# Kernel tuning notes

Hardware: AMD Instinct MI355X
Metric: run time of the kernel (lower is better)

The kernel has to match this reference:

```python
import jax, jax.numpy as jnp
import numpy as np
from jax import lax

B, C, H, W = 8, 512, 16, 16
Di, N, R, K = 1024, 16, 32, 4  # d_inner, d_state, dt_rank, num scan directions
EPS = 1e-5


def _ln(x, g, b):
    mu = x.mean(-1, keepdims=True)
    var = ((x - mu) ** 2).mean(-1, keepdims=True)
    return (x - mu) * lax.rsqrt(var + EPS) * g + b


def _ss2d_core(xc, x_proj_w, dt_w, dt_b, A_logs, Ds):
    # xc: (b, Di, H, W) after depthwise conv + SiLU. 4-direction selective scan.
    b = xc.shape[0]
    L = H * W
    x_flat = xc.reshape(b, Di, L)
    x_wh = xc.transpose(0, 1, 3, 2).reshape(b, Di, L)
    x_hwwh = jnp.stack([x_flat, x_wh], 1)                  # (b,2,Di,L)
    xs = jnp.concatenate([x_hwwh, x_hwwh[..., ::-1]], 1)   # (b,K,Di,L)
    x_dbl = jnp.einsum('bkdl,kcd->bkcl', xs, x_proj_w)     # (b,K,R+2N,L)
    dts, Bs, Cs = x_dbl[:, :, :R], x_dbl[:, :, R:R + N], x_dbl[:, :, R + N:]
    dts = jnp.einsum('bkrl,kdr->bkdl', dts, dt_w)
    delta = jax.nn.softplus(dts + dt_b[None, :, :, None])  # (b,K,Di,L)
    A = -jnp.exp(A_logs).reshape(K, Di, N)                 # (K,Di,N)

    def step(h, inp):
        d, u, Bl, Cl = inp  # d,u:(b,K,Di)  Bl,Cl:(b,K,N)
        h = jnp.exp(d[..., None] * A) * h + (d * u)[..., None] * Bl[:, :, None, :]
        yl = jnp.einsum('bkdn,bkn->bkd', h, Cl)
        return h, yl

    inps = (delta.transpose(3, 0, 1, 2), xs.transpose(3, 0, 1, 2),
            Bs.transpose(3, 0, 1, 2), Cs.transpose(3, 0, 1, 2))
    h0 = jnp.zeros((b, K, Di, N), xc.dtype)
    _, ys = lax.scan(step, h0, inps)                       # (L,b,K,Di)
    ys = ys.transpose(1, 2, 3, 0) + xs * Ds.reshape(1, K, Di, 1)  # + D*u skip
    inv = ys[:, 2:4, :, ::-1]
    wh = ys[:, 1].reshape(b, Di, W, H).transpose(0, 1, 3, 2).reshape(b, Di, L)
    invwh = inv[:, 1].reshape(b, Di, W, H).transpose(0, 1, 3, 2).reshape(b, Di, L)
    y = ys[:, 0] + inv[:, 0] + wh + invwh                  # (b,Di,L)
    return y.transpose(0, 2, 1).reshape(b, H, W, Di)


def _conv_ffn(x, ffn_conv_w, bn_g, bn_b, bn_mean, bn_var, fc1_w, fc2_w):
    x = lax.conv_general_dilated(x, ffn_conv_w, (1, 1), [(1, 1), (1, 1)],
                                 dimension_numbers=('NCHW', 'OIHW', 'NCHW'))
    x = ((x - bn_mean[:, None, None]) * lax.rsqrt(bn_var + EPS)[:, None, None]
         * bn_g[:, None, None] + bn_b[:, None, None])
    x = jnp.clip(x, 0.0, 6.0)                              # ReLU6
    x = jnp.einsum('bchw,oc->bohw', x, fc1_w)              # 1x1 conv fc1
    x = jax.nn.gelu(x, approximate=False)
    return jnp.einsum('bchw,oc->bohw', x, fc2_w)           # 1x1 conv fc2


def _forward(x, y, ln1_g, ln1_b, in_proj_w, conv_w, conv_b, x_proj_w, dt_w,
             dt_b, A_logs, Ds, out_norm_g, out_norm_b, out_proj_w, ffn_conv_w,
             bn_g, bn_b, bn_mean, bn_var, fc1_w, fc2_w, lin1_w, lin1_b,
             lin2_w, lin2_b):
    # --- VSSBlock: LN -> SS2D -> residual ---
    x1 = x.transpose(0, 2, 3, 1)                           # (B,H,W,C)
    xn = _ln(x1, ln1_g, ln1_b)
    xz = jnp.einsum('bhwc,oc->bhwo', xn, in_proj_w)        # in_proj (no bias)
    xa, z = xz[..., :Di], xz[..., Di:]
    xc = xa.transpose(0, 3, 1, 2)                          # (B,Di,H,W)
    xc = lax.conv_general_dilated(xc, conv_w, (1, 1), [(1, 1), (1, 1)],
                                  feature_group_count=Di,
                                  dimension_numbers=('NCHW', 'OIHW', 'NCHW'))
    xc = jax.nn.silu(xc + conv_b[:, None, None])
    yc = _ss2d_core(xc, x_proj_w, dt_w, dt_b, A_logs, Ds)  # (B,H,W,Di)
    yc = _ln(yc, out_norm_g, out_norm_b) * jax.nn.silu(z)
    vss = x1 + jnp.einsum('bhwd,od->bhwo', yc, out_proj_w)
    # --- ConvFFN ---
    xm = _conv_ffn(vss.transpose(0, 3, 1, 2), ffn_conv_w, bn_g, bn_b, bn_mean,
                   bn_var, fc1_w, fc2_w)                   # (B,C,H,W)
    # --- channel attention: both pools are AdaptiveAvgPool2d(1), so max==avg ---
    pooled = y.mean(axis=(2, 3))                           # (B,C)
    lin = jax.nn.relu(pooled @ lin1_w.T + lin1_b) @ lin2_w.T + lin2_b
    gate = jax.nn.sigmoid(2.0 * lin)                       # linear_max + linear_avg
    return gate[:, :, None, None] * xm


def setup_inputs() -> dict:
    key = jax.random.key(0)
    ks = jax.random.split(key, 16)
    n = lambda i, shape, s=0.05: jax.random.normal(ks[i], shape, jnp.float32) * s
    return {
        'x': n(0, (B, C, H, W), 1.0),
        'y': n(1, (B, C, H, W), 1.0),
        'ln1_g': jnp.ones((C,), jnp.float32), 'ln1_b': jnp.zeros((C,), jnp.float32),
        'in_proj_w': n(2, (2 * Di, C)),
        'conv_w': n(3, (Di, 1, 3, 3), 0.2), 'conv_b': jnp.zeros((Di,), jnp.float32),
        'x_proj_w': n(4, (K, R + 2 * N, Di)),
        'dt_w': n(5, (K, Di, R), 0.1), 'dt_b': n(6, (K, Di), 0.1),
        'A_logs': n(7, (K * Di, N), 0.1), 'Ds': jnp.ones((K * Di,), jnp.float32),
        'out_norm_g': jnp.ones((Di,), jnp.float32), 'out_norm_b': jnp.zeros((Di,), jnp.float32),
        'out_proj_w': n(8, (C, Di)),
        'ffn_conv_w': n(9, (C, C, 3, 3)),
        'bn_g': jnp.ones((C,), jnp.float32), 'bn_b': jnp.zeros((C,), jnp.float32),
        'bn_mean': jnp.zeros((C,), jnp.float32), 'bn_var': jnp.ones((C,), jnp.float32),
        'fc1_w': n(10, (C, C)), 'fc2_w': n(11, (C, C)),
        'lin1_w': n(12, (C // 2, C)), 'lin1_b': jnp.zeros((C // 2,), jnp.float32),
        'lin2_w': n(13, (C, C // 2)), 'lin2_b': jnp.zeros((C,), jnp.float32),
    }


def reference(x, y, ln1_g, ln1_b, in_proj_w, conv_w, conv_b, x_proj_w, dt_w,
              dt_b, A_logs, Ds, out_norm_g, out_norm_b, out_proj_w, ffn_conv_w,
              bn_g, bn_b, bn_mean, bn_var, fc1_w, fc2_w, lin1_w, lin1_b,
              lin2_w, lin2_b):
    return _forward(x, y, ln1_g, ln1_b, in_proj_w, conv_w, conv_b, x_proj_w,
                    dt_w, dt_b, A_logs, Ds, out_norm_g, out_norm_b, out_proj_w,
                    ffn_conv_w, bn_g, bn_b, bn_mean, bn_var, fc1_w, fc2_w,
                    lin1_w, lin1_b, lin2_w, lin2_b)
```

## Files before the change

kernel.cpp:

```cpp
#include <hip/hip_runtime.h>
#include <hip/hip_bf16.h>
#include <math.h>

#define DEV_INLINE __device__ __forceinline__

constexpr int B_ = 8, C_ = 512, L_ = 256;
constexpr float EPS_ = 1e-5f;

typedef __attribute__((ext_vector_type(8))) short bf16x8;
typedef __attribute__((ext_vector_type(4))) float f32x4;

DEV_INLINE int lmap1(int l) { return ((l & 15) << 4) | (l >> 4); }
DEV_INLINE float sigmoidf_(float x) { return 1.f / (1.f + __expf(-x)); }
DEV_INLINE float siluf_(float x) { return x * sigmoidf_(x); }
DEV_INLINE float ex2_(float x) { return __builtin_amdgcn_exp2f(x); }

DEV_INLINE unsigned pk2(float a, float b) {
    __hip_bfloat16 x = __float2bfloat16(a), y = __float2bfloat16(b);
    unsigned short ux = *reinterpret_cast<unsigned short*>(&x);
    unsigned short uy = *reinterpret_cast<unsigned short*>(&y);
    return ((unsigned)uy << 16) | ux;
}

__global__ __launch_bounds__(256) void k_pool(const float* __restrict__ y, float* __restrict__ pooled) {
    int bc = blockIdx.x;
    int t = threadIdx.x;
    __shared__ float red[256];
    red[t] = y[bc * 256 + t];
    __syncthreads();
    for (int s = 128; s > 0; s >>= 1) { if (t < s) red[t] += red[t + s]; __syncthreads(); }
    if (t == 0) pooled[bc] = red[0] * (1.f / 256.f);
}

__global__ __launch_bounds__(256) void k_gate(const float* __restrict__ pooled,
                                              const float* __restrict__ lin1_w, const float* __restrict__ lin1_b,
                                              const float* __restrict__ lin2_w, const float* __restrict__ lin2_b,
                                              float* __restrict__ gate) {
    int b = blockIdx.x;
    int t = threadIdx.x;
    __shared__ float p[512];
    __shared__ float h1[256];
    p[t] = pooled[b * 512 + t];
    p[t + 256] = pooled[b * 512 + t + 256];
    __syncthreads();
    float s = lin1_b[t];
    const float4* wp1 = (const float4*)(lin1_w + t * 512);
    #pragma unroll 4
    for (int c = 0; c < 128; ++c) {
        float4 pv = *(const float4*)(p + c * 4);
        float4 wv = wp1[c];
        s = fmaf(pv.x, wv.x, s); s = fmaf(pv.y, wv.y, s);
        s = fmaf(pv.z, wv.z, s); s = fmaf(pv.w, wv.w, s);
    }
    h1[t] = fmaxf(s, 0.f);
    __syncthreads();
    #pragma unroll
    for (int cc = 0; cc < 2; ++cc) {
        int c = t + cc * 256;
        float s2 = lin2_b[c];
        const float4* wp2 = (const float4*)(lin2_w + c * 256);
        #pragma unroll 4
        for (int j = 0; j < 64; ++j) {
            float4 hv = *(const float4*)(h1 + j * 4);
            float4 wv = wp2[j];
            s2 = fmaf(hv.x, wv.x, s2); s2 = fmaf(hv.y, wv.y, s2);
            s2 = fmaf(hv.z, wv.z, s2); s2 = fmaf(hv.w, wv.w, s2);
        }
        gate[b * 512 + c] = sigmoidf_(2.f * s2);
    }
}

__global__ __launch_bounds__(256) void k_ln(const float* __restrict__ x, const float* __restrict__ g,
                                            const float* __restrict__ bta, __hip_bfloat16* __restrict__ xnb) {
    int pos = blockIdx.x;
    int b = pos >> 8, l = pos & 255;
    int t = threadIdx.x;
    float v0 = x[(b * C_ + t) * L_ + l];
    float v1 = x[(b * C_ + t + 256) * L_ + l];
    __shared__ float red[256];
    red[t] = v0 + v1;
    __syncthreads();
    for (int s = 128; s > 0; s >>= 1) { if (t < s) red[t] += red[t + s]; __syncthreads(); }
    float mu = red[0] * (1.f / 512.f);
    __syncthreads();
    float d0 = v0 - mu, d1 = v1 - mu;
    red[t] = d0 * d0 + d1 * d1;
    __syncthreads();
    for (int s = 128; s > 0; s >>= 1) { if (t < s) red[t] += red[t + s]; __syncthreads(); }
    float rs = rsqrtf(red[0] * (1.f / 512.f) + EPS_);
    xnb[pos * C_ + t] = __float2bfloat16(d0 * rs * g[t] + bta[t]);
    xnb[pos * C_ + t + 256] = __float2bfloat16(d1 * rs * g[t + 256] + bta[t + 256]);
}

__global__ __launch_bounds__(256) void k_wcast6(const float* __restrict__ ip, const float* __restrict__ xp,
                                                const float* __restrict__ op, const float* __restrict__ f1,
                                                const float* __restrict__ f2, const float* __restrict__ dtw,
                                                const float* __restrict__ fw, __hip_bfloat16* __restrict__ dst) {
    if (blockIdx.x < 2432) {
        size_t e = ((size_t)blockIdx.x * 256 + threadIdx.x) * 4;
        const float* src; size_t off;
        if (e < 1048576) { src = ip; off = e; }
        else if (e < 1310720) { src = xp; off = e - 1048576; }
        else if (e < 1835008) { src = op; off = e - 1310720; }
        else if (e < 2097152) { src = f1; off = e - 1835008; }
        else if (e < 2359296) { src = f2; off = e - 2097152; }
        else { src = dtw; off = e - 2359296; }
        float4 v = *(const float4*)(src + off);
        uint2 o; o.x = pk2(v.x, v.y); o.y = pk2(v.z, v.w);
        *(uint2*)(dst + e) = o;
    } else {
        int gid = (blockIdx.x - 2432) * 256 + threadIdx.x;
        __hip_bfloat16* wt = dst + 2490368;
        const float* src = fw + (size_t)gid * 9;
        #pragma unroll
        for (int tap = 0; tap < 9; ++tap) wt[(size_t)tap * 262144 + gid] = __float2bfloat16(src[tap]);
    }
}

enum { M_INPROJ = 0, M_XDBL = 1, M_OUTPROJ = 2, M_FC1 = 3, M_FC2 = 4, M_DELTA = 5 };

template <int MODE>
__global__ __launch_bounds__(256) void gemm_mfma(const void* __restrict__ Aptr, const __hip_bfloat16* __restrict__ Wb,
                                                 float* __restrict__ O, float* __restrict__ O2,
                                                 const float* __restrict__ AUX, __hip_bfloat16* __restrict__ Ob) {
    constexpr int KK = (MODE == M_XDBL || MODE == M_OUTPROJ) ? 1024 : (MODE == M_DELTA) ? 32 : 512;
    constexpr bool A_COPY = (MODE == M_INPROJ || MODE == M_OUTPROJ || MODE == M_FC1 || MODE == M_FC2);
    __shared__ short Asm[64 * 32];
    __shared__ short Bsm[64 * 32];
    const int t = threadIdx.x;
    const int lane = t & 63, wv = t >> 6;
    int m0, n0 = 0, kdir = 0, bq = 0;
    if constexpr (MODE == M_XDBL) { m0 = blockIdx.x * 64; kdir = blockIdx.y; }
    else if constexpr (MODE == M_FC2) { bq = blockIdx.x >> 3; m0 = (blockIdx.x & 7) * 64; n0 = blockIdx.y * 64; }
    else { m0 = blockIdx.x * 64; n0 = blockIdx.y * 64; }
    const int kdel = (m0 >> 8) & 3;

    const int r_ = t >> 2, kq = t & 3;
    const int skey = (r_ >> 1) & 3;
    uint4* adst = (uint4*)(Asm + r_ * 32) + (kq ^ skey);
    uint4* bdst = (uint4*)(Bsm + r_ * 32) + (kq ^ skey);

    const float* arowf = nullptr;
    const __hip_bfloat16* arowb = nullptr;
    if constexpr (MODE == M_INPROJ) arowb = (const __hip_bfloat16*)Aptr + (size_t)(m0 + r_) * 512 + kq * 8;
    else if constexpr (MODE == M_XDBL) {
        int m = m0 + r_; int b = m >> 8, l = m & 255;
        int lm = (kdir < 2) ? l : 255 - l;
        arowf = (const float*)Aptr + (size_t)((b * 2 + (kdir & 1)) * 256 + lm) * 1024 + kq * 8;
    } else if constexpr (MODE == M_OUTPROJ) arowb = (const __hip_bfloat16*)Aptr + (size_t)(m0 + r_) * 1024 + kq * 8;
    else if constexpr (MODE == M_FC1) arowb = (const __hip_bfloat16*)Aptr + (size_t)(m0 + r_) * 512 + kq * 8;
    else if constexpr (MODE == M_DELTA) arowf = (const float*)Aptr + (size_t)(m0 + r_) * 64 + kq * 8;
    else arowb = Wb + (size_t)(m0 + r_) * 512 + kq * 8;

    const __hip_bfloat16* browb = nullptr;
    if constexpr (MODE == M_INPROJ) browb = Wb + (size_t)(n0 + r_) * 512 + kq * 8;
    else if constexpr (MODE == M_XDBL) browb = Wb + (size_t)(kdir * 64 + r_) * 1024 + kq * 8;
    else if constexpr (MODE == M_OUTPROJ) browb = Wb + (size_t)(n0 + r_) * 1024 + kq * 8;
    else if constexpr (MODE == M_FC1) browb = Wb + (size_t)(n0 + r_) * 512 + kq * 8;
    else if constexpr (MODE == M_DELTA) browb = Wb + ((size_t)(kdel * 1024 + n0 + r_)) * 32 + kq * 8;
    else browb = (const __hip_bfloat16*)Aptr + (size_t)(bq * 256 + n0 + r_) * 512 + kq * 8;

    f32x4 acc[4];
    #pragma unroll
    for (int nf = 0; nf < 4; ++nf) acc[nf] = (f32x4){0.f, 0.f, 0.f, 0.f};

    for (int k0 = 0; k0 < KK; k0 += 32) {
        __syncthreads();
        if constexpr (A_COPY) {
            *adst = *(const uint4*)(arowb + k0);
        } else {
            float4 u0 = *(const float4*)(arowf + k0);
            float4 u1 = *(const float4*)(arowf + k0 + 4);
            uint4 pk; pk.x = pk2(u0.x, u0.y); pk.y = pk2(u0.z, u0.w); pk.z = pk2(u1.x, u1.y); pk.w = pk2(u1.z, u1.w);
            *adst = pk;
        }
        *bdst = *(const uint4*)(browb + k0);
        __syncthreads();
        int mrow = wv * 16 + (lane & 15);
        int ks = lane >> 4;
        bf16x8 af = *(const bf16x8*)(Asm + mrow * 32 + ((ks ^ ((mrow >> 1) & 3)) * 8));
        #pragma unroll
        for (int nf = 0; nf < 4; ++nf) {
            int nrow = nf * 16 + (lane & 15);
            bf16x8 bfv = *(const bf16x8*)(Bsm + nrow * 32 + ((ks ^ ((nrow >> 1) & 3)) * 8));
            acc[nf] = __builtin_amdgcn_mfma_f32_16x16x32_bf16(af, bfv, acc[nf], 0, 0, 0);
        }
    }

    const int mlb = (lane >> 4) * 4, nl = lane & 15;
    #pragma unroll
    for (int nf = 0; nf < 4; ++nf) {
        #pragma unroll
        for (int j = 0; j < 4; ++j) {
            float v = acc[nf][j];
            int m_loc = wv * 16 + mlb + j;
            int n_loc = nf * 16 + nl;
            if constexpr (MODE == M_INPROJ) {
                int m = m0 + m_loc, n = n0 + n_loc;
                if (n0 < 1024) O[(size_t)m * 1024 + n] = v;
                else O2[(size_t)m * 1024 + (n - 1024)] = v;
            } else if constexpr (MODE == M_XDBL) {
                int m = m0 + m_loc; int b = m >> 8, l = m & 255;
                O[((size_t)(b * 4 + kdir) * 256 + l) * 64 + n_loc] = v;
            } else if constexpr (MODE == M_OUTPROJ) {
                int m = m0 + m_loc, n = n0 + n_loc; int b = m >> 8, l = m & 255;
                float f = AUX[((size_t)b * 512 + n) * 256 + l] + v;
                Ob[(size_t)m * 512 + n] = __float2bfloat16(f);
            } else if constexpr (MODE == M_FC1) {
                int m = m0 + m_loc, n = n0 + n_loc;
                float gl = 0.5f * v * (1.f + erff(v * 0.70710678118f));
                Ob[(size_t)m * 512 + n] = __float2bfloat16(gl);
            } else if constexpr (MODE == M_DELTA) {
                int m = m0 + m_loc, n = n0 + n_loc;
                int bkk = m >> 8, l = m & 255;
                float v2 = v + AUX[kdel * 1024 + n];
                float dlt = (v2 > 20.f) ? v2 : __logf(1.f + __expf(v2));
                O[((((size_t)bkk * 32) + (n >> 5)) * 256 + l) * 32 + (n & 31)] = dlt;
            } else {
                int c = m0 + m_loc, n = n0 + n_loc;
                O[((size_t)(bq * 512 + c)) * 256 + n] = v * AUX[bq * 512 + c];
            }
        }
    }
}

__global__ __launch_bounds__(256) void k_dwconv2(const float* __restrict__ xa, const float* __restrict__ cw,
                                                 const float* __restrict__ cb, float* __restrict__ xs_t) {
    int pos = blockIdx.x;
    int b = pos >> 8, l = pos & 255;
    int h = l >> 4, w = l & 15;
    int t = threadIdx.x;
    int d = t * 4;
    float wv[36];
    {
        const float4* cp = (const float4*)(cw + (size_t)d * 9);
        #pragma unroll
        for (int j = 0; j < 9; ++j) { float4 v = cp[j]; wv[j*4] = v.x; wv[j*4+1] = v.y; wv[j*4+2] = v.z; wv[j*4+3] = v.w; }
    }
    float4 bias = *(const float4*)(cb + d);
    float a0 = bias.x, a1 = bias.y, a2 = bias.z, a3 = bias.w;
    #pragma unroll
    for (int ky = -1; ky <= 1; ++ky) {
        int hh = h + ky;
        if ((unsigned)hh >= 16u) continue;
        #pragma unroll
        for (int kx = -1; kx <= 1; ++kx) {
            int ww = w + kx;
            if ((unsigned)ww >= 16u) continue;
            float4 v = *(const float4*)(xa + (size_t)(b * 256 + hh * 16 + ww) * 1024 + d);
            int tap = (ky + 1) * 3 + (kx + 1);
            a0 = fmaf(v.x, wv[0 * 9 + tap], a0);
            a1 = fmaf(v.y, wv[1 * 9 + tap], a1);
            a2 = fmaf(v.z, wv[2 * 9 + tap], a2);
            a3 = fmaf(v.w, wv[3 * 9 + tap], a3);
        }
    }
    float4 o; o.x = siluf_(a0); o.y = siluf_(a1); o.z = siluf_(a2); o.w = siluf_(a3);
    *(float4*)(xs_t + ((size_t)(b * 2 + 0) * 256 + l) * 1024 + d) = o;
    *(float4*)(xs_t + ((size_t)(b * 2 + 1) * 256 + lmap1(l)) * 1024 + d) = o;
}

__global__ __launch_bounds__(512) void k_scan7(const float* __restrict__ xs_t, const float* __restrict__ x_dbl,
                                               const float* __restrict__ A_logs, const float* __restrict__ Ds,
                                               float* __restrict__ dys) {
    const int bk = blockIdx.x >> 5;
    const int db = blockIdx.x & 31;
    const int b = bk >> 2, k = bk & 3;
    const int t = threadIdx.x;
    const int c = t >> 5, dd = t & 31;
    const int d = db * 32 + dd;
    const bool rev = (k >= 2);

    __shared__ float Ssh[16][33];
    __shared__ float locH[16][32][17];

    float An2[16];
    {
        const float* alp = A_logs + (size_t)(k * 1024 + d) * 16;
        #pragma unroll
        for (int i = 0; i < 16; ++i) An2[i] = -__expf(alp[i]) * 1.44269504088896f;
    }
    const float Dv = Ds[k * 1024 + d];

    const int lbeg = c * 16;
    float* yp = dys + (((size_t)bk * 32 + db) * 256 + lbeg) * 32 + dd;
    const float* up = xs_t + ((size_t)(b * 2 + (k & 1)) * 256 + (rev ? 255 - lbeg : lbeg)) * 1024 + d;
    const ptrdiff_t ustr = rev ? -1024 : 1024;
    const float* xc = x_dbl + (size_t)bk * 256 * 64 + lbeg * 64;

    float h[16];
    #pragma unroll
    for (int i = 0; i < 16; ++i) h[i] = 0.f;
    float S = 0.f;

    #pragma unroll 4
    for (int li = 0; li < 16; ++li) {
        float dl = yp[li * 32];
        float u = up[(ptrdiff_t)li * ustr];
        S += dl;
        float du = dl * u;
        #pragma unroll
        for (int q = 0; q < 4; ++q) {
            float4 Bq = *(const float4*)(xc + li * 64 + 32 + q * 4);
            h[q*4+0] = fmaf(ex2_(dl * An2[q*4+0]), h[q*4+0], du * Bq.x);
            h[q*4+1] = fmaf(ex2_(dl * An2[q*4+1]), h[q*4+1], du * Bq.y);
            h[q*4+2] = fmaf(ex2_(dl * An2[q*4+2]), h[q*4+2], du * Bq.z);
            h[q*4+3] = fmaf(ex2_(dl * An2[q*4+3]), h[q*4+3], du * Bq.w);
        }
    }
    Ssh[c][dd] = S;
    #pragma unroll
    for (int i = 0; i < 16; ++i) locH[c][dd][i] = h[i];
    __syncthreads();

    #pragma unroll
    for (int i = 0; i < 16; ++i) h[i] = 0.f;
    for (int j = 0; j < c; ++j) {
        float Sj = Ssh[j][dd];
        #pragma unroll
        for (int i = 0; i < 16; ++i) h[i] = fmaf(ex2_(Sj * An2[i]), h[i], locH[j][dd][i]);
    }

    #pragma unroll 4
    for (int li = 0; li < 16; ++li) {
        float dl = yp[li * 32];
        float u = up[(ptrdiff_t)li * ustr];
        float du = dl * u;
        float yv = 0.f;
        #pragma unroll
        for (int q = 0; q < 4; ++q) {
            float4 Bq = *(const float4*)(xc + li * 64 + 32 + q * 4);
            float4 Cq = *(const float4*)(xc + li * 64 + 48 + q * 4);
            h[q*4+0] = fmaf(ex2_(dl * An2[q*4+0]), h[q*4+0], du * Bq.x); yv = fmaf(h[q*4+0], Cq.x, yv);
            h[q*4+1] = fmaf(ex2_(dl * An2[q*4+1]), h[q*4+1], du * Bq.y); yv = fmaf(h[q*4+1], Cq.y, yv);
            h[q*4+2] = fmaf(ex2_(dl * An2[q*4+2]), h[q*4+2], du * Bq.z); yv = fmaf(h[q*4+2], Cq.z, yv);
            h[q*4+3] = fmaf(ex2_(dl * An2[q*4+3]), h[q*4+3], du * Bq.w); yv = fmaf(h[q*4+3], Cq.w, yv);
        }
        yp[li * 32] = yv + u * Dv;
    }
}

__global__ __launch_bounds__(256) void k_combine(const float* __restrict__ dys, const float* __restrict__ z,
                                                 const float* __restrict__ g, const float* __restrict__ bb,
                                                 __hip_bfloat16* __restrict__ ycb) {
    int pos = blockIdx.x;
    int b = pos >> 8, l = pos & 255;
    int t = threadIdx.x;
    int lw = lmap1(l);
    int db0 = t >> 5, dd = t & 31;
    float v[4];
    float psum = 0.f;
    #pragma unroll
    for (int q = 0; q < 4; ++q) {
        int dbq = db0 + q * 8;
        float s0 = dys[((((size_t)(b * 4 + 0) * 32) + dbq) * 256 + l) * 32 + dd];
        float s1 = dys[((((size_t)(b * 4 + 1) * 32) + dbq) * 256 + lw) * 32 + dd];
        float s2 = dys[((((size_t)(b * 4 + 2) * 32) + dbq) * 256 + (255 - l)) * 32 + dd];
        float s3 = dys[((((size_t)(b * 4 + 3) * 32) + dbq) * 256 + (255 - lw)) * 32 + dd];
        v[q] = s0 + s1 + s2 + s3;
        psum += v[q];
    }
    __shared__ float red[256];
    red[t] = psum;
    __syncthreads();
    for (int s = 128; s > 0; s >>= 1) { if (t < s) red[t] += red[t + s]; __syncthreads(); }
    float mu = red[0] * (1.f / 1024.f);
    __syncthreads();
    float p2 = 0.f;
    #pragma unroll
    for (int q = 0; q < 4; ++q) { float ddv = v[q] - mu; p2 += ddv * ddv; }
    red[t] = p2;
    __syncthreads();
    for (int s = 128; s > 0; s >>= 1) { if (t < s) red[t] += red[t + s]; __syncthreads(); }
    float rs = rsqrtf(red[0] * (1.f / 1024.f) + EPS_);
    #pragma unroll
    for (int q = 0; q < 4; ++q) {
        int d = (db0 + q * 8) * 32 + dd;
        float zn = z[(size_t)pos * 1024 + d];
        float o = ((v[q] - mu) * rs * g[d] + bb[d]) * siluf_(zn);
        ycb[(size_t)pos * 1024 + d] = __float2bfloat16(o);
    }
}

__global__ __launch_bounds__(256) void k_conv2m(const __hip_bfloat16* __restrict__ vssb,
                                                const __hip_bfloat16* __restrict__ wt,
                                                float* __restrict__ convp) {
    __shared__ short Asm[18 * 18 * 32];
    __shared__ short Bsm[9 * 64 * 32];
    const int b = blockIdx.x, co0 = blockIdx.y * 64, split = blockIdx.z;
    const int t = threadIdx.x;
    const int lane = t & 63, wid = t >> 6;
    const int wcol = lane & 15, slot = lane >> 4;

    f32x4 acc[4][4];
    #pragma unroll
    for (int r = 0; r < 4; ++r)
        #pragma unroll
        for (int g = 0; g < 4; ++g) acc[r][g] = (f32x4){0.f, 0.f, 0.f, 0.f};

    for (int ch = 0; ch < 2; ++ch) {
        const int ci0 = split * 64 + ch * 32;
        __syncthreads();
        for (int i = t; i < 324; i += 256) {
            int row = i / 18, col = i - row * 18;
            uint4 v0 = {0,0,0,0}, v1 = {0,0,0,0}, v2 = {0,0,0,0}, v3 = {0,0,0,0};
            if (row >= 1 && row <= 16 && col >= 1 && col <= 16) {
                const uint4* src = (const uint4*)(vssb + ((size_t)(b * 256 + (row - 1) * 16 + (col - 1)) * 512 + ci0));
                v0 = src[0]; v1 = src[1]; v2 = src[2]; v3 = src[3];
            }
            uint4* dst = (uint4*)(Asm + i * 32);
            int key = (col >> 1) & 3;
            dst[0 ^ key] = v0; dst[1 ^ key] = v1; dst[2 ^ key] = v2; dst[3 ^ key] = v3;
        }
        for (int i = t; i < 576; i += 256) {
            int tap = i >> 6, col = i & 63;
            const uint4* src = (const uint4*)(wt + ((size_t)(tap * 512 + co0 + col) * 512 + ci0));
            uint4* dst = (uint4*)(Bsm + i * 32);
            int key = (col >> 1) & 3;
            dst[0 ^ key] = src[0]; dst[1 ^ key] = src[1]; dst[2 ^ key] = src[2]; dst[3 ^ key] = src[3];
        }
        __syncthreads();
        #pragma unroll
        for (int tap = 0; tap < 9; ++tap) {
            const int ky = tap / 3, kx = tap - ky * 3;
            bf16x8 af[4], bfr[4];
            #pragma unroll
            for (int r = 0; r < 4; ++r) {
                int crow = wid * 4 + r + ky;
                int ccol = wcol + kx;
                int s2 = slot ^ ((ccol >> 1) & 3);
                af[r] = *(const bf16x8*)(Asm + ((crow * 18 + ccol) * 32 + s2 * 8));
            }
            #pragma unroll
            for (int g = 0; g < 4; ++g) {
                int col = g * 16 + wcol;
                int s2 = slot ^ ((col >> 1) & 3);
                bfr[g] = *(const bf16x8*)(Bsm + ((tap * 64 + col) * 32 + s2 * 8));
            }
            #pragma unroll
            for (int r = 0; r < 4; ++r)
                #pragma unroll
                for (int g = 0; g < 4; ++g)
                    acc[r][g] = __builtin_amdgcn_mfma_f32_16x16x32_bf16(af[r], bfr[g], acc[r][g], 0, 0, 0);
        }
    }
    float* base = convp + (size_t)split * 1048576 + (size_t)b * 512 * 256;
    #pragma unroll
    for (int r = 0; r < 4; ++r) {
        int h = wid * 4 + r;
        #pragma unroll
        for (int g = 0; g < 4; ++g) {
            int co = co0 + g * 16 + wcol;
            *(f32x4*)(base + (size_t)co * 256 + h * 16 + slot * 4) = acc[r][g];
        }
    }
}

__global__ __launch_bounds__(256) void k_convred2(const float* __restrict__ convp,
                                                  const float* __restrict__ bn_g, const float* __restrict__ bn_b,
                                                  const float* __restrict__ bn_mean, const float* __restrict__ bn_var,
                                                  __hip_bfloat16* __restrict__ t1b) {
    int b = blockIdx.x >> 7, cb = (blockIdx.x >> 3) & 15, pb = blockIdx.x & 7;
    int co0 = cb * 32, pos0 = pb * 32;
    int t = threadIdx.x;
    int ti = t >> 5, tj = t & 31;
    __shared__ float tile[32][33];
    #pragma unroll
    for (int r = 0; r < 4; ++r) {
        int co = co0 + ti + r * 8;
        size_t idx = ((size_t)b * 512 + co) * 256 + pos0 + tj;
        float s = 0.f;
        #pragma unroll
        for (int sp = 0; sp < 8; ++sp) s += convp[idx + (size_t)sp * 1048576];
        float o = (s - bn_mean[co]) * rsqrtf(bn_var[co] + EPS_) * bn_g[co] + bn_b[co];
        tile[ti + r * 8][tj] = fminf(fmaxf(o, 0.f), 6.f);
    }
    __syncthreads();
    #pragma unroll
    for (int r = 0; r < 4; ++r) {
        int pos = pos0 + ti + r * 8;
        t1b[((size_t)b * 256 + pos) * 512 + co0 + tj] = __float2bfloat16(tile[tj][ti + r * 8]);
    }
}

extern "C" void kernel_launch(void* const* d_in, const int* in_sizes, int n_in,
                              void* d_out, int out_size, void* d_ws, size_t ws_size,
                              hipStream_t stream) {
    const float* x = (const float*)d_in[0];
    const float* y = (const float*)d_in[1];
    const float* ln1_g = (const float*)d_in[2];
    const float* ln1_b = (const float*)d_in[3];
    const float* in_proj_w = (const float*)d_in[4];
    const float* conv_w = (const float*)d_in[5];
    const float* conv_b = (const float*)d_in[6];
    const float* x_proj_w = (const float*)d_in[7];
    const float* dt_w = (const float*)d_in[8];
    const float* dt_b = (const float*)d_in[9];
    const float* A_logs = (const float*)d_in[10];
    const float* Ds = (const float*)d_in[11];
    const float* out_norm_g = (const float*)d_in[12];
    const float* out_norm_b = (const float*)d_in[13];
    const float* out_proj_w = (const float*)d_in[14];
    const float* ffn_conv_w = (const float*)d_in[15];
    const float* bn_g = (const float*)d_in[16];
    const float* bn_b = (const float*)d_in[17];
    const float* bn_mean = (const float*)d_in[18];
    const float* bn_var = (const float*)d_in[19];
    const float* fc1_w = (const float*)d_in[20];
    const float* fc2_w = (const float*)d_in[21];
    const float* lin1_w = (const float*)d_in[22];
    const float* lin1_b = (const float*)d_in[23];
    const float* lin2_w = (const float*)d_in[24];
    const float* lin2_b = (const float*)d_in[25];
    float* out = (float*)d_out;

    char* ws = (char*)d_ws;
    size_t off = 0;
    auto alloc = [&](size_t nf) { float* p = (float*)(ws + off); off += nf * sizeof(float); return p; };
    float* xn    = alloc(2048u * 512);
    float* xa    = alloc(2048u * 1024);
    float* z     = alloc(2048u * 1024);
    float* xs_t  = alloc(2u * 2048 * 1024);
    float* x_dbl = alloc(8u * 4 * 256 * 64);
    float* ys_t  = alloc(4u * 2048 * 1024);
    float* wb    = alloc(2424832);
    float* pooled = alloc(4096);
    float* gate   = alloc(4096);

    __hip_bfloat16* xnb = (__hip_bfloat16*)xn;
    __hip_bfloat16* vssb = (__hip_bfloat16*)xn;
    __hip_bfloat16* ycb = (__hip_bfloat16*)xa;
    __hip_bfloat16* t1b = (__hip_bfloat16*)xs_t;
    __hip_bfloat16* t2b = (__hip_bfloat16*)(xs_t + 2048u * 512);
    float* convp = ys_t;
    __hip_bfloat16* inprojb = (__hip_bfloat16*)wb;
    __hip_bfloat16* xprojb  = inprojb + 1048576;
    __hip_bfloat16* outprojb = xprojb + 262144;
    __hip_bfloat16* fc1b = outprojb + 524288;
    __hip_bfloat16* fc2b = fc1b + 262144;
    __hip_bfloat16* dtwb = fc2b + 262144;
    __hip_bfloat16* w_t  = dtwb + 131072;

    k_wcast6<<<3456, 256, 0, stream>>>(in_proj_w, x_proj_w, out_proj_w, fc1_w, fc2_w, dt_w, ffn_conv_w, inprojb);
    k_pool<<<4096, 256, 0, stream>>>(y, pooled);
    k_gate<<<8, 256, 0, stream>>>(pooled, lin1_w, lin1_b, lin2_w, lin2_b, gate);
    k_ln<<<2048, 256, 0, stream>>>(x, ln1_g, ln1_b, xnb);
    gemm_mfma<M_INPROJ><<<dim3(32, 32), 256, 0, stream>>>(xnb, inprojb, xa, z, nullptr, nullptr);
    k_dwconv2<<<2048, 256, 0, stream>>>(xa, conv_w, conv_b, xs_t);
    gemm_mfma<M_XDBL><<<dim3(32, 4), 256, 0, stream>>>(xs_t, xprojb, x_dbl, nullptr, nullptr, nullptr);
    gemm_mfma<M_DELTA><<<dim3(128, 16), 256, 0, stream>>>(x_dbl, dtwb, ys_t, nullptr, dt_b, nullptr);
    k_scan7<<<1024, 512, 0, stream>>>(xs_t, x_dbl, A_logs, Ds, ys_t);
    k_combine<<<2048, 256, 0, stream>>>(ys_t, z, out_norm_g, out_norm_b, ycb);
    gemm_mfma<M_OUTPROJ><<<dim3(32, 8), 256, 0, stream>>>(ycb, outprojb, nullptr, nullptr, x, vssb);
    k_conv2m<<<dim3(8, 8, 8), 256, 0, stream>>>(vssb, w_t, convp);
    k_convred2<<<1024, 256, 0, stream>>>(convp, bn_g, bn_b, bn_mean, bn_var, t1b);
    gemm_mfma<M_FC1><<<dim3(32, 8), 256, 0, stream>>>(t1b, fc1b, nullptr, nullptr, nullptr, t2b);
    gemm_mfma<M_FC2><<<dim3(64, 4), 256, 0, stream>>>(t2b, fc2b, out, nullptr, gate, nullptr);
}
```

Baseline: 247.2 us.

## Store inproj/dwconv intermediates in bf16 and merge prologue kernels into one launch

The in-projection outputs (xa, z) and the depthwise-conv output xs are now stored as bf16 instead of fp32. Every downstream consumer (dwconv, the x_dbl GEMM which now copies A directly, scan, combine) reads the half-width data, which halves that memory traffic. Separately, the weight cast, LayerNorm, pooling and gate MLP kernels are merged into a single prologue launch, and the pooling is folded into the gate blocks. This removes launches and the pooled buffer, but it adds bf16 rounding error to the activations and lets 8 gate blocks each read y serially.

```diff
diff --git a/kernel.cpp b/kernel.cpp
--- a/kernel.cpp
+++ b/kernel.cpp
@@ -14,6 +14,7 @@
 DEV_INLINE float sigmoidf_(float x) { return 1.f / (1.f + __expf(-x)); }
 DEV_INLINE float siluf_(float x) { return x * sigmoidf_(x); }
 DEV_INLINE float ex2_(float x) { return __builtin_amdgcn_exp2f(x); }
+DEV_INLINE float b2f(__hip_bfloat16 v) { return __bfloat162float(v); }
 
 DEV_INLINE unsigned pk2(float a, float b) {
     __hip_bfloat16 x = __float2bfloat16(a), y = __float2bfloat16(b);
@@ -22,82 +23,21 @@
     return ((unsigned)uy << 16) | ux;
 }
 
-__global__ __launch_bounds__(256) void k_pool(const float* __restrict__ y, float* __restrict__ pooled) {
-    int bc = blockIdx.x;
-    int t = threadIdx.x;
-    __shared__ float red[256];
-    red[t] = y[bc * 256 + t];
-    __syncthreads();
-    for (int s = 128; s > 0; s >>= 1) { if (t < s) red[t] += red[t + s]; __syncthreads(); }
-    if (t == 0) pooled[bc] = red[0] * (1.f / 256.f);
-}
-
-__global__ __launch_bounds__(256) void k_gate(const float* __restrict__ pooled,
-                                              const float* __restrict__ lin1_w, const float* __restrict__ lin1_b,
-                                              const float* __restrict__ lin2_w, const float* __restrict__ lin2_b,
-                                              float* __restrict__ gate) {
-    int b = blockIdx.x;
-    int t = threadIdx.x;
-    __shared__ float p[512];
-    __shared__ float h1[256];
-    p[t] = pooled[b * 512 + t];
-    p[t + 256] = pooled[b * 512 + t + 256];
-    __syncthreads();
-    float s = lin1_b[t];
-    const float4* wp1 = (const float4*)(lin1_w + t * 512);
-    #pragma unroll 4
-    for (int c = 0; c < 128; ++c) {
-        float4 pv = *(const float4*)(p + c * 4);
-        float4 wv = wp1[c];
-        s = fmaf(pv.x, wv.x, s); s = fmaf(pv.y, wv.y, s);
-        s = fmaf(pv.z, wv.z, s); s = fmaf(pv.w, wv.w, s);
-    }
-    h1[t] = fmaxf(s, 0.f);
-    __syncthreads();
-    #pragma unroll
-    for (int cc = 0; cc < 2; ++cc) {
-        int c = t + cc * 256;
-        float s2 = lin2_b[c];
-        const float4* wp2 = (const float4*)(lin2_w + c * 256);
-        #pragma unroll 4
-        for (int j = 0; j < 64; ++j) {
-            float4 hv = *(const float4*)(h1 + j * 4);
-            float4 wv = wp2[j];
-            s2 = fmaf(hv.x, wv.x, s2); s2 = fmaf(hv.y, wv.y, s2);
-            s2 = fmaf(hv.z, wv.z, s2); s2 = fmaf(hv.w, wv.w, s2);
-        }
-        gate[b * 512 + c] = sigmoidf_(2.f * s2);
-    }
-}
-
-__global__ __launch_bounds__(256) void k_ln(const float* __restrict__ x, const float* __restrict__ g,
-                                            const float* __restrict__ bta, __hip_bfloat16* __restrict__ xnb) {
-    int pos = blockIdx.x;
-    int b = pos >> 8, l = pos & 255;
-    int t = threadIdx.x;
-    float v0 = x[(b * C_ + t) * L_ + l];
-    float v1 = x[(b * C_ + t + 256) * L_ + l];
-    __shared__ float red[256];
-    red[t] = v0 + v1;
-    __syncthreads();
-    for (int s = 128; s > 0; s >>= 1) { if (t < s) red[t] += red[t + s]; __syncthreads(); }
-    float mu = red[0] * (1.f / 512.f);
-    __syncthreads();
-    float d0 = v0 - mu, d1 = v1 - mu;
-    red[t] = d0 * d0 + d1 * d1;
-    __syncthreads();
-    for (int s = 128; s > 0; s >>= 1) { if (t < s) red[t] += red[t + s]; __syncthreads(); }
-    float rs = rsqrtf(red[0] * (1.f / 512.f) + EPS_);
-    xnb[pos * C_ + t] = __float2bfloat16(d0 * rs * g[t] + bta[t]);
-    xnb[pos * C_ + t + 256] = __float2bfloat16(d1 * rs * g[t + 256] + bta[t + 256]);
-}
-
-__global__ __launch_bounds__(256) void k_wcast6(const float* __restrict__ ip, const float* __restrict__ xp,
-                                                const float* __restrict__ op, const float* __restrict__ f1,
-                                                const float* __restrict__ f2, const float* __restrict__ dtw,
-                                                const float* __restrict__ fw, __hip_bfloat16* __restrict__ dst) {
-    if (blockIdx.x < 2432) {
-        size_t e = ((size_t)blockIdx.x * 256 + threadIdx.x) * 4;
+__global__ __launch_bounds__(256) void k_prologue(const float* __restrict__ ip, const float* __restrict__ xp,
+                                                  const float* __restrict__ op, const float* __restrict__ f1,
+                                                  const float* __restrict__ f2, const float* __restrict__ dtw,
+                                                  const float* __restrict__ fw, __hip_bfloat16* __restrict__ dst,
+                                                  const float* __restrict__ x, const float* __restrict__ ln_g,
+                                                  const float* __restrict__ ln_b, __hip_bfloat16* __restrict__ xnb,
+                                                  const float* __restrict__ y,
+                                                  const float* __restrict__ lin1_w, const float* __restrict__ lin1_b,
+                                                  const float* __restrict__ lin2_w, const float* __restrict__ lin2_b,
+                                                  float* __restrict__ gate) {
+    const int bid = blockIdx.x;
+    const int t = threadIdx.x;
+    __shared__ float sh[768];
+    if (bid < 2432) {
+        size_t e = ((size_t)bid * 256 + t) * 4;
         const float* src; size_t off;
         if (e < 1048576) { src = ip; off = e; }
         else if (e < 1310720) { src = xp; off = e - 1048576; }
@@ -108,12 +48,69 @@
         float4 v = *(const float4*)(src + off);
         uint2 o; o.x = pk2(v.x, v.y); o.y = pk2(v.z, v.w);
         *(uint2*)(dst + e) = o;
-    } else {
-        int gid = (blockIdx.x - 2432) * 256 + threadIdx.x;
+    } else if (bid < 3456) {
+        int gid = (bid - 2432) * 256 + t;
         __hip_bfloat16* wt = dst + 2490368;
         const float* src = fw + (size_t)gid * 9;
         #pragma unroll
         for (int tap = 0; tap < 9; ++tap) wt[(size_t)tap * 262144 + gid] = __float2bfloat16(src[tap]);
+    } else if (bid < 5504) {
+        int pos = bid - 3456;
+        int b = pos >> 8, l = pos & 255;
+        float v0 = x[(b * C_ + t) * L_ + l];
+        float v1 = x[(b * C_ + t + 256) * L_ + l];
+        float* red = sh;
+        red[t] = v0 + v1;
+        __syncthreads();
+        for (int s = 128; s > 0; s >>= 1) { if (t < s) red[t] += red[t + s]; __syncthreads(); }
+        float mu = red[0] * (1.f / 512.f);
+        __syncthreads();
+        float d0 = v0 - mu, d1 = v1 - mu;
+        red[t] = d0 * d0 + d1 * d1;
+        __syncthreads();
+        for (int s = 128; s > 0; s >>= 1) { if (t < s) red[t] += red[t + s]; __syncthreads(); }
+        float rs = rsqrtf(red[0] * (1.f / 512.f) + EPS_);
+        xnb[pos * C_ + t] = __float2bfloat16(d0 * rs * ln_g[t] + ln_b[t]);
+        xnb[pos * C_ + t + 256] = __float2bfloat16(d1 * rs * ln_g[t + 256] + ln_b[t + 256]);
+    } else {
+        int b = bid - 5504;
+        float* p = sh;
+        float* h1 = sh + 512;
+        #pragma unroll
+        for (int cc = 0; cc < 2; ++cc) {
+            int cch = t + cc * 256;
+            const float4* yp = (const float4*)(y + (size_t)(b * 512 + cch) * 256);
+            float s = 0.f;
+            #pragma unroll 4
+            for (int j = 0; j < 64; ++j) { float4 v = yp[j]; s += v.x + v.y + v.z + v.w; }
+            p[cch] = s * (1.f / 256.f);
+        }
+        __syncthreads();
+        float s = lin1_b[t];
+        const float4* wp1 = (const float4*)(lin1_w + t * 512);
+        #pragma unroll 4
+        for (int c = 0; c < 128; ++c) {
+            float4 pv = *(const float4*)(p + c * 4);
+            float4 wv = wp1[c];
+            s = fmaf(pv.x, wv.x, s); s = fmaf(pv.y, wv.y, s);
+            s = fmaf(pv.z, wv.z, s); s = fmaf(pv.w, wv.w, s);
+        }
+        h1[t] = fmaxf(s, 0.f);
+        __syncthreads();
+        #pragma unroll
+        for (int cc = 0; cc < 2; ++cc) {
+            int c = t + cc * 256;
+            float s2 = lin2_b[c];
+            const float4* wp2 = (const float4*)(lin2_w + c * 256);
+            #pragma unroll 4
+            for (int j = 0; j < 64; ++j) {
+                float4 hv = *(const float4*)(h1 + j * 4);
+                float4 wv = wp2[j];
+                s2 = fmaf(hv.x, wv.x, s2); s2 = fmaf(hv.y, wv.y, s2);
+                s2 = fmaf(hv.z, wv.z, s2); s2 = fmaf(hv.w, wv.w, s2);
+            }
+            gate[b * 512 + c] = sigmoidf_(2.f * s2);
+        }
     }
 }
 
@@ -124,7 +121,7 @@
                                                  float* __restrict__ O, float* __restrict__ O2,
                                                  const float* __restrict__ AUX, __hip_bfloat16* __restrict__ Ob) {
     constexpr int KK = (MODE == M_XDBL || MODE == M_OUTPROJ) ? 1024 : (MODE == M_DELTA) ? 32 : 512;
-    constexpr bool A_COPY = (MODE == M_INPROJ || MODE == M_OUTPROJ || MODE == M_FC1 || MODE == M_FC2);
+    constexpr bool A_COPY = (MODE != M_DELTA);
     __shared__ short Asm[64 * 32];
     __shared__ short Bsm[64 * 32];
     const int t = threadIdx.x;
@@ -146,7 +143,7 @@
     else if constexpr (MODE == M_XDBL) {
         int m = m0 + r_; int b = m >> 8, l = m & 255;
         int lm = (kdir < 2) ? l : 255 - l;
-        arowf = (const float*)Aptr + (size_t)((b * 2 + (kdir & 1)) * 256 + lm) * 1024 + kq * 8;
+        arowb = (const __hip_bfloat16*)Aptr + (size_t)((b * 2 + (kdir & 1)) * 256 + lm) * 1024 + kq * 8;
     } else if constexpr (MODE == M_OUTPROJ) arowb = (const __hip_bfloat16*)Aptr + (size_t)(m0 + r_) * 1024 + kq * 8;
     else if constexpr (MODE == M_FC1) arowb = (const __hip_bfloat16*)Aptr + (size_t)(m0 + r_) * 512 + kq * 8;
     else if constexpr (MODE == M_DELTA) arowf = (const float*)Aptr + (size_t)(m0 + r_) * 64 + kq * 8;
@@ -197,8 +194,8 @@
             int n_loc = nf * 16 + nl;
             if constexpr (MODE == M_INPROJ) {
                 int m = m0 + m_loc, n = n0 + n_loc;
-                if (n0 < 1024) O[(size_t)m * 1024 + n] = v;
-                else O2[(size_t)m * 1024 + (n - 1024)] = v;
+                if (n0 < 1024) Ob[(size_t)m * 1024 + n] = __float2bfloat16(v);
+                else ((__hip_bfloat16*)O2)[(size_t)m * 1024 + (n - 1024)] = __float2bfloat16(v);
             } else if constexpr (MODE == M_XDBL) {
                 int m = m0 + m_loc; int b = m >> 8, l = m & 255;
                 O[((size_t)(b * 4 + kdir) * 256 + l) * 64 + n_loc] = v;
@@ -224,8 +221,8 @@
     }
 }
 
-__global__ __launch_bounds__(256) void k_dwconv2(const float* __restrict__ xa, const float* __restrict__ cw,
-                                                 const float* __restrict__ cb, float* __restrict__ xs_t) {
+__global__ __launch_bounds__(256) void k_dwconv2(const __hip_bfloat16* __restrict__ xab, const float* __restrict__ cw,
+                                                 const float* __restrict__ cb, __hip_bfloat16* __restrict__ xsb) {
     int pos = blockIdx.x;
     int b = pos >> 8, l = pos & 255;
     int h = l >> 4, w = l & 15;
@@ -247,20 +244,21 @@
         for (int kx = -1; kx <= 1; ++kx) {
             int ww = w + kx;
             if ((unsigned)ww >= 16u) continue;
-            float4 v = *(const float4*)(xa + (size_t)(b * 256 + hh * 16 + ww) * 1024 + d);
+            uint2 rv = *(const uint2*)(xab + (size_t)(b * 256 + hh * 16 + ww) * 1024 + d);
+            const __hip_bfloat16* pv = (const __hip_bfloat16*)&rv;
             int tap = (ky + 1) * 3 + (kx + 1);
-            a0 = fmaf(v.x, wv[0 * 9 + tap], a0);
-            a1 = fmaf(v.y, wv[1 * 9 + tap], a1);
-            a2 = fmaf(v.z, wv[2 * 9 + tap], a2);
-            a3 = fmaf(v.w, wv[3 * 9 + tap], a3);
-        }
-    }
-    float4 o; o.x = siluf_(a0); o.y = siluf_(a1); o.z = siluf_(a2); o.w = siluf_(a3);
-    *(float4*)(xs_t + ((size_t)(b * 2 + 0) * 256 + l) * 1024 + d) = o;
-    *(float4*)(xs_t + ((size_t)(b * 2 + 1) * 256 + lmap1(l)) * 1024 + d) = o;
-}
-
-__global__ __launch_bounds__(512) void k_scan7(const float* __restrict__ xs_t, const float* __restrict__ x_dbl,
+            a0 = fmaf(b2f(pv[0]), wv[0 * 9 + tap], a0);
+            a1 = fmaf(b2f(pv[1]), wv[1 * 9 + tap], a1);
+            a2 = fmaf(b2f(pv[2]), wv[2 * 9 + tap], a2);
+            a3 = fmaf(b2f(pv[3]), wv[3 * 9 + tap], a3);
+        }
+    }
+    uint2 ov; ov.x = pk2(siluf_(a0), siluf_(a1)); ov.y = pk2(siluf_(a2), siluf_(a3));
+    *(uint2*)(xsb + ((size_t)(b * 2 + 0) * 256 + l) * 1024 + d) = ov;
+    *(uint2*)(xsb + ((size_t)(b * 2 + 1) * 256 + lmap1(l)) * 1024 + d) = ov;
+}
+
+__global__ __launch_bounds__(512) void k_scan7(const __hip_bfloat16* __restrict__ xsb, const float* __restrict__ x_dbl,
                                                const float* __restrict__ A_logs, const float* __restrict__ Ds,
                                                float* __restrict__ dys) {
     const int bk = blockIdx.x >> 5;
@@ -284,7 +282,7 @@
 
     const int lbeg = c * 16;
     float* yp = dys + (((size_t)bk * 32 + db) * 256 + lbeg) * 32 + dd;
-    const float* up = xs_t + ((size_t)(b * 2 + (k & 1)) * 256 + (rev ? 255 - lbeg : lbeg)) * 1024 + d;
+    const __hip_bfloat16* up = xsb + ((size_t)(b * 2 + (k & 1)) * 256 + (rev ? 255 - lbeg : lbeg)) * 1024 + d;
     const ptrdiff_t ustr = rev ? -1024 : 1024;
     const float* xc = x_dbl + (size_t)bk * 256 * 64 + lbeg * 64;
 
@@ -296,7 +294,7 @@
     #pragma unroll 4
     for (int li = 0; li < 16; ++li) {
         float dl = yp[li * 32];
-        float u = up[(ptrdiff_t)li * ustr];
+        float u = b2f(up[(ptrdiff_t)li * ustr]);
         S += dl;
         float du = dl * u;
         #pragma unroll
@@ -324,7 +322,7 @@
     #pragma unroll 4
     for (int li = 0; li < 16; ++li) {
         float dl = yp[li * 32];
-        float u = up[(ptrdiff_t)li * ustr];
+        float u = b2f(up[(ptrdiff_t)li * ustr]);
         float du = dl * u;
         float yv = 0.f;
         #pragma unroll
@@ -340,7 +338,7 @@
     }
 }
 
-__global__ __launch_bounds__(256) void k_combine(const float* __restrict__ dys, const float* __restrict__ z,
+__global__ __launch_bounds__(256) void k_combine(const float* __restrict__ dys, const __hip_bfloat16* __restrict__ zb,
                                                  const float* __restrict__ g, const float* __restrict__ bb,
                                                  __hip_bfloat16* __restrict__ ycb) {
     int pos = blockIdx.x;
@@ -376,7 +374,7 @@
     #pragma unroll
     for (int q = 0; q < 4; ++q) {
         int d = (db0 + q * 8) * 32 + dd;
-        float zn = z[(size_t)pos * 1024 + d];
+        float zn = b2f(zb[(size_t)pos * 1024 + d]);
         float o = ((v[q] - mu) * rs * g[d] + bb[d]) * siluf_(zn);
         ycb[(size_t)pos * 1024 + d] = __float2bfloat16(o);
     }
@@ -524,12 +522,14 @@
     float* x_dbl = alloc(8u * 4 * 256 * 64);
     float* ys_t  = alloc(4u * 2048 * 1024);
     float* wb    = alloc(2424832);
-    float* pooled = alloc(4096);
-    float* gate   = alloc(4096);
+    float* gate  = alloc(4096);
 
     __hip_bfloat16* xnb = (__hip_bfloat16*)xn;
     __hip_bfloat16* vssb = (__hip_bfloat16*)xn;
+    __hip_bfloat16* xab = (__hip_bfloat16*)xa;
     __hip_bfloat16* ycb = (__hip_bfloat16*)xa;
+    __hip_bfloat16* zb  = (__hip_bfloat16*)z;
+    __hip_bfloat16* xsb = (__hip_bfloat16*)xs_t;
     __hip_bfloat16* t1b = (__hip_bfloat16*)xs_t;
     __hip_bfloat16* t2b = (__hip_bfloat16*)(xs_t + 2048u * 512);
     float* convp = ys_t;
@@ -541,16 +541,14 @@
     __hip_bfloat16* dtwb = fc2b + 262144;
     __hip_bfloat16* w_t  = dtwb + 131072;
 
-    k_wcast6<<<3456, 256, 0, stream>>>(in_proj_w, x_proj_w, out_proj_w, fc1_w, fc2_w, dt_w, ffn_conv_w, inprojb);
-    k_pool<<<4096, 256, 0, stream>>>(y, pooled);
-    k_gate<<<8, 256, 0, stream>>>(pooled, lin1_w, lin1_b, lin2_w, lin2_b, gate);
-    k_ln<<<2048, 256, 0, stream>>>(x, ln1_g, ln1_b, xnb);
-    gemm_mfma<M_INPROJ><<<dim3(32, 32), 256, 0, stream>>>(xnb, inprojb, xa, z, nullptr, nullptr);
-    k_dwconv2<<<2048, 256, 0, stream>>>(xa, conv_w, conv_b, xs_t);
-    gemm_mfma<M_XDBL><<<dim3(32, 4), 256, 0, stream>>>(xs_t, xprojb, x_dbl, nullptr, nullptr, nullptr);
+    k_prologue<<<5512, 256, 0, stream>>>(in_proj_w, x_proj_w, out_proj_w, fc1_w, fc2_w, dt_w, ffn_conv_w,
+                                         inprojb, x, ln1_g, ln1_b, xnb, y, lin1_w, lin1_b, lin2_w, lin2_b, gate);
+    gemm_mfma<M_INPROJ><<<dim3(32, 32), 256, 0, stream>>>(xnb, inprojb, nullptr, (float*)zb, nullptr, xab);
+    k_dwconv2<<<2048, 256, 0, stream>>>(xab, conv_w, conv_b, xsb);
+    gemm_mfma<M_XDBL><<<dim3(32, 4), 256, 0, stream>>>(xsb, xprojb, x_dbl, nullptr, nullptr, nullptr);
     gemm_mfma<M_DELTA><<<dim3(128, 16), 256, 0, stream>>>(x_dbl, dtwb, ys_t, nullptr, dt_b, nullptr);
-    k_scan7<<<1024, 512, 0, stream>>>(xs_t, x_dbl, A_logs, Ds, ys_t);
-    k_combine<<<2048, 256, 0, stream>>>(ys_t, z, out_norm_g, out_norm_b, ycb);
+    k_scan7<<<1024, 512, 0, stream>>>(xsb, x_dbl, A_logs, Ds, ys_t);
+    k_combine<<<2048, 256, 0, stream>>>(ys_t, zb, out_norm_g, out_norm_b, ycb);
     gemm_mfma<M_OUTPROJ><<<dim3(32, 8), 256, 0, stream>>>(ycb, outprojb, nullptr, nullptr, x, vssb);
     k_conv2m<<<dim3(8, 8, 8), 256, 0, stream>>>(vssb, w_t, convp);
     k_convred2<<<1024, 256, 0, stream>>>(convp, bn_g, bn_b, bn_mean, bn_var, t1b);
```

Measured after the change: 244.5 us. About the same (-1.1%).
